# Performance work log

Hardware: AMD Instinct MI355X
Metric: run time of the kernel (lower is better)

## Reference

```python
import jax, jax.numpy as jnp
import numpy as np

DEPTH = 8
INPUT_WIDTH = 64
INNER_WIDTH = 32
BATCH = 65536
N_NODES = 2 ** DEPTH - 1   # 255 inner nodes
N_LEAVES = 2 ** DEPTH      # 256 bins
EPS = 1e-8


def _tree_paths(depth):
    """For each leaf, the inner-node index at each level and whether the path
    goes right (right child uses 1 - decision, mirroring hstack([p, 1-p]) indexing)."""
    node_idx = np.zeros((2 ** depth, depth), dtype=np.int32)
    is_right = np.zeros((2 ** depth, depth), dtype=bool)
    for leaf in range(2 ** depth):
        idx = 0
        for level in range(depth):
            bit = (leaf >> (depth - 1 - level)) & 1
            node_idx[leaf, level] = idx
            is_right[leaf, level] = bool(bit)
            idx = 2 * idx + 1 + bit
    return node_idx, is_right

_NODE_IDX_NP, _IS_RIGHT_NP = _tree_paths(DEPTH)
NODE_IDX = jnp.asarray(_NODE_IDX_NP)   # [L, depth]
IS_RIGHT = jnp.asarray(_IS_RIGHT_NP)   # [L, depth]


def _init_b_i():
    """Replicates PartialRadialLayer.init_tree_weights: thresholds evenly dividing [0,1],
    stored as logits so sigmoid(b_i) recovers the threshold."""
    b = np.zeros(N_NODES, dtype=np.float64)
    b[0] = -0.5
    used = 1
    for i in range(1, DEPTH):
        n_nodes = 2 ** i
        div = float(2 ** (i + 1))
        for node in range(n_nodes):
            b[used + node] = -(2 * node + 1) / div
        used += n_nodes
    return np.log(-b / (1.0 + b)).astype(np.float32).reshape(1, -1)


def setup_inputs() -> dict:
    key = jax.random.key(0)
    kx, kr, kt = jax.random.split(key, 3)
    x = jax.random.normal(kx, (BATCH, INPUT_WIDTH), dtype=jnp.float32)
    # kaiming_normal_ on [1, input_width]: fan_in = input_width
    ray = jax.random.normal(kr, (1, INPUT_WIDTH), dtype=jnp.float32) * np.sqrt(2.0 / INPUT_WIDTH)
    # kaiming_normal_ on [L, I, W]: fan_in = I * W
    inner_transforms = jax.random.normal(kt, (N_LEAVES, INPUT_WIDTH, INNER_WIDTH), dtype=jnp.float32) * np.sqrt(2.0 / (INPUT_WIDTH * INNER_WIDTH))
    w_i = jnp.zeros((1, N_NODES), dtype=jnp.float32)
    a_i = 5.0 * jnp.ones((1, N_NODES), dtype=jnp.float32)
    b_i = jnp.asarray(_init_b_i())
    return {"x": x, "ray": ray, "inner_transforms": inner_transforms,
            "w_i": w_i, "b_i": b_i, "a_i": a_i}


def reference(x, ray, inner_transforms, w_i, b_i, a_i):
    # angles: arccos(cosine_similarity(x, ray)) / pi
    x_norm = jnp.maximum(jnp.linalg.norm(x, axis=1), EPS)            # [B]
    r_norm = jnp.maximum(jnp.linalg.norm(ray, axis=1), EPS)          # [1]
    cos = jnp.clip((x @ ray[0]) / (x_norm * r_norm), -1.0, 1.0)      # [B]
    angles = jnp.arccos(cos) / jnp.pi                                # [B]

    # per-node decisions
    node_fns = (0.5 + jax.nn.sigmoid(w_i)) * angles[:, None] - jax.nn.sigmoid(b_i)  # [B, N]
    decisions = jax.nn.sigmoid(node_fns * (1.0 + a_i))                               # [B, N]

    # soft bin distribution: product along each root-to-leaf path
    g = decisions[:, NODE_IDX]                       # [B, L, depth]
    vals = jnp.where(IS_RIGHT, 1.0 - g, g)           # right child -> 1 - p
    distribution = jnp.prod(vals, axis=2)            # [B, L]

    # weighted per-leaf transforms: einsum('bi,liw->blw') then ('bl,blo->bo'), fused
    out = jnp.einsum('bl,bi,liw->bw', distribution, x, inner_transforms)
    return out
```

## Files before the change

kernel.cpp:

```cpp
#include <hip/hip_runtime.h>
#include <hip/hip_bf16.h>

#define NLEAF 256
#define MBLK 256
#define THREADS 256

typedef __attribute__((ext_vector_type(4))) float f32x4;
typedef __attribute__((ext_vector_type(4))) unsigned int uint4v;
typedef __attribute__((ext_vector_type(8))) __bf16 bf16x8;
typedef __attribute__((ext_vector_type(4))) __bf16 bf16x4;

#define OFF_DIST 0
#define OFF_XP   131072
#define OFF_AC   147456
#define OFF_BC   148480
#define OFF_ANG  149504
#define OFF_RAY  150528
#define SMEM_BYTES 150784

__device__ __forceinline__ float sigf(float s) { return 1.0f / (1.0f + __expf(-s)); }

__global__ __launch_bounds__(256) void prep_T(const float* __restrict__ T,
                                              __bf16* __restrict__ wsT) {
  __shared__ char tile[4096];
  const int l = blockIdx.x;
  const float* src = T + (size_t)l * 2048;
  const int t = threadIdx.x;
#pragma unroll
  for (int p = 0; p < 2; ++p) {
    int e = p * 1024 + t * 4;
    f32x4 v = *(const f32x4*)(src + e);
    int k = e >> 5, w0 = e & 31;
#pragma unroll
    for (int j = 0; j < 4; ++j) {
      int w = w0 + j;
      int off = ((k >> 5) * 2 + (w >> 4)) * 1024 +
                (((k >> 3) & 3) * 16 + (w & 15)) * 16 + (k & 7) * 2;
      *(__bf16*)(tile + off) = (__bf16)v[j];
    }
  }
  __syncthreads();
  *(uint4v*)((char*)wsT + (size_t)l * 4096 + t * 16) = *(const uint4v*)(tile + t * 16);
}

template <bool USE_WS>
__global__ __launch_bounds__(THREADS, 1)
void prl_main(const float* __restrict__ x, const float* __restrict__ ray,
              const float* __restrict__ w_i, const float* __restrict__ b_i,
              const float* __restrict__ a_i, const void* __restrict__ tsrc,
              float* __restrict__ out) {
  extern __shared__ char smem[];
  const int tid = threadIdx.x;
  const int lane = tid & 63;
  const int wid = tid >> 6;
  const int g = lane >> 4;
  const int ln = lane & 15;
  const int row0 = blockIdx.x * MBLK;

  float* A_c = (float*)(smem + OFF_AC);
  float* B_c = (float*)(smem + OFF_BC);
  float* angles = (float*)(smem + OFF_ANG);
  float* ray_l = (float*)(smem + OFF_RAY);
  __bf16* distb = (__bf16*)(smem + OFF_DIST);

  if (tid < 255) {
    float aa = 1.0f + a_i[tid];
    A_c[tid] = (0.5f + sigf(w_i[tid])) * aa;
    B_c[tid] = -sigf(b_i[tid]) * aa;
  }
  if (tid < 64) ray_l[tid] = ray[tid];
  __syncthreads();

  bf16x8 afrag[4][2] = {};
  float* xp = (float*)(smem + OFF_XP);
  for (int c = 0; c < 4; ++c) {
    const float* xg = x + (size_t)(row0 + c * 64) * 64;
#pragma unroll
    for (int p = 0; p < 4; ++p) {
      int idx = p * 256 + tid;
      f32x4 v = *(const f32x4*)(xg + idx * 4);
      *(f32x4*)(xp + idx * 4) = v;
      int cg = idx & 15;
      f32x4 rv = *(const f32x4*)(ray_l + cg * 4);
      float a0 = v[0] * v[0] + v[1] * v[1] + v[2] * v[2] + v[3] * v[3];
      float a1 = v[0] * rv[0] + v[1] * rv[1] + v[2] * rv[2] + v[3] * rv[3];
      float a2 = rv[0] * rv[0] + rv[1] * rv[1] + rv[2] * rv[2] + rv[3] * rv[3];
#pragma unroll
      for (int s = 1; s < 16; s <<= 1) {
        a0 += __shfl_xor(a0, s, 64);
        a1 += __shfl_xor(a1, s, 64);
        a2 += __shfl_xor(a2, s, 64);
      }
      if ((tid & 15) == 0) {
        int r = idx >> 4;
        float xn = fmaxf(sqrtf(a0), 1e-8f);
        float rn = fmaxf(sqrtf(a2), 1e-8f);
        float cs = a1 / (xn * rn);
        cs = fminf(fmaxf(cs, -1.0f), 1.0f);
        angles[c * 64 + r] = acosf(cs) * 0.31830988618379067f;
      }
    }
    __syncthreads();
    if (wid == c) {
#pragma unroll
      for (int mt = 0; mt < 4; ++mt)
#pragma unroll
        for (int kt = 0; kt < 2; ++kt) {
          int rl = mt * 16 + ln;
          int k0 = kt * 32 + g * 8;
          f32x4 u0 = *(const f32x4*)(xp + rl * 64 + k0);
          f32x4 u1 = *(const f32x4*)(xp + rl * 64 + k0 + 4);
          bf16x8 af;
          af[0] = (__bf16)u0[0]; af[1] = (__bf16)u0[1];
          af[2] = (__bf16)u0[2]; af[3] = (__bf16)u0[3];
          af[4] = (__bf16)u1[0]; af[5] = (__bf16)u1[1];
          af[6] = (__bf16)u1[2]; af[7] = (__bf16)u1[3];
          afrag[mt][kt] = af;
        }
    }
    __syncthreads();
  }

  __bf16* PA = (__bf16*)(smem + OFF_XP);
  __bf16* PB = (__bf16*)(smem + OFF_XP + 8192);
  {
    float ang = angles[tid];
    float d = sigf(fmaf(A_c[0], ang, B_c[0]));
    PA[tid] = (__bf16)d;
    PA[256 + tid] = (__bf16)(1.0f - d);
  }
  __syncthreads();
#pragma unroll
  for (int it = 0; it < 2; ++it) {
    int e = it * 256 + tid;
    int n = e >> 8, r = e & 255;
    float p = (float)PA[e];
    float ang = angles[r];
    float d = sigf(fmaf(A_c[1 + n], ang, B_c[1 + n]));
    PB[(2 * n) * 256 + r] = (__bf16)(p * d);
    PB[(2 * n + 1) * 256 + r] = (__bf16)(p * (1.0f - d));
  }
  __syncthreads();
#pragma unroll
  for (int it = 0; it < 4; ++it) {
    int e = it * 256 + tid;
    int n = e >> 8, r = e & 255;
    float p = (float)PB[e];
    float ang = angles[r];
    float d = sigf(fmaf(A_c[3 + n], ang, B_c[3 + n]));
    PA[(2 * n) * 256 + r] = (__bf16)(p * d);
    PA[(2 * n + 1) * 256 + r] = (__bf16)(p * (1.0f - d));
  }
  __syncthreads();
#pragma unroll
  for (int it = 0; it < 8; ++it) {
    int e = it * 256 + tid;
    int n = e >> 8, r = e & 255;
    float p = (float)PA[e];
    float ang = angles[r];
    float d = sigf(fmaf(A_c[7 + n], ang, B_c[7 + n]));
    PB[(2 * n) * 256 + r] = (__bf16)(p * d);
    PB[(2 * n + 1) * 256 + r] = (__bf16)(p * (1.0f - d));
  }
  __syncthreads();
#pragma unroll
  for (int it = 0; it < 16; ++it) {
    int e = it * 256 + tid;
    int n4 = e >> 8, r = e & 255;
    float p4 = (float)PB[e];
    float ang = angles[r];
    float d4 = sigf(fmaf(A_c[15 + n4], ang, B_c[15 + n4]));
    float p5[2] = {p4 * d4, p4 * (1.0f - d4)};
#pragma unroll
    for (int b5 = 0; b5 < 2; ++b5) {
      int n5 = 2 * n4 + b5;
      float d5 = sigf(fmaf(A_c[31 + n5], ang, B_c[31 + n5]));
      float p6[2] = {p5[b5] * d5, p5[b5] * (1.0f - d5)};
#pragma unroll
      for (int b6 = 0; b6 < 2; ++b6) {
        int n6 = 2 * n5 + b6;
        float d6 = sigf(fmaf(A_c[63 + n6], ang, B_c[63 + n6]));
        float p7[2] = {p6[b6] * d6, p6[b6] * (1.0f - d6)};
#pragma unroll
        for (int b7 = 0; b7 < 2; ++b7) {
          int n7 = 2 * n6 + b7;
          float d7 = sigf(fmaf(A_c[127 + n7], ang, B_c[127 + n7]));
          float pv = p7[b7];
          distb[(2 * n7) * 256 + r] = (__bf16)(pv * d7);
          distb[(2 * n7 + 1) * 256 + r] = (__bf16)(pv * (1.0f - d7));
        }
      }
    }
  }
  __syncthreads();

  f32x4 acc[4][2] = {};
  const char* bp = (const char*)tsrc + lane * 16;

  auto step = [&](const bf16x8 (&bv)[4], int l) {
    f32x4 dv[4];
#pragma unroll
    for (int mt = 0; mt < 4; ++mt) {
      bf16x4 dd = *(const bf16x4*)(distb + l * 256 + wid * 64 + mt * 16 + g * 4);
      dv[mt] = (f32x4){(float)dd[0], (float)dd[1], (float)dd[2], (float)dd[3]};
    }
    f32x4 zero = {0.0f, 0.0f, 0.0f, 0.0f};
#pragma unroll
    for (int mt = 0; mt < 4; ++mt)
#pragma unroll
      for (int nt = 0; nt < 2; ++nt) {
        bf16x8 bk0, bk1;
        if constexpr (USE_WS) {
          bk0 = bv[nt];
          bk1 = bv[2 + nt];
        } else {
          const float* tp0 = (const float*)tsrc + (size_t)l * 2048 + (g * 8) * 32 + nt * 16 + ln;
          const float* tp1 = tp0 + 32 * 32;
#pragma unroll
          for (int j = 0; j < 8; ++j) {
            bk0[j] = (__bf16)tp0[j * 32];
            bk1[j] = (__bf16)tp1[j * 32];
          }
        }
        f32x4 y = __builtin_amdgcn_mfma_f32_16x16x32_bf16(afrag[mt][0], bk0, zero, 0, 0, 0);
        y = __builtin_amdgcn_mfma_f32_16x16x32_bf16(afrag[mt][1], bk1, y, 0, 0, 0);
        acc[mt][nt] += dv[mt] * y;
      }
  };

  if constexpr (USE_WS) {
    bf16x8 b0[4], b1[4], b2[4], b3[4];
#pragma unroll
    for (int f = 0; f < 4; ++f) {
      b0[f] = *(const bf16x8*)(bp + 0 * 4096 + f * 1024);
      b1[f] = *(const bf16x8*)(bp + 1 * 4096 + f * 1024);
      b2[f] = *(const bf16x8*)(bp + 2 * 4096 + f * 1024);
      b3[f] = *(const bf16x8*)(bp + 3 * 4096 + f * 1024);
    }
    for (int l = 0; l < NLEAF; l += 4) {
      step(b0, l);
      if (l + 4 < NLEAF) {
        const char* q = bp + (size_t)(l + 4) * 4096;
#pragma unroll
        for (int f = 0; f < 4; ++f) b0[f] = *(const bf16x8*)(q + f * 1024);
      }
      step(b1, l + 1);
      if (l + 5 < NLEAF) {
        const char* q = bp + (size_t)(l + 5) * 4096;
#pragma unroll
        for (int f = 0; f < 4; ++f) b1[f] = *(const bf16x8*)(q + f * 1024);
      }
      step(b2, l + 2);
      if (l + 6 < NLEAF) {
        const char* q = bp + (size_t)(l + 6) * 4096;
#pragma unroll
        for (int f = 0; f < 4; ++f) b2[f] = *(const bf16x8*)(q + f * 1024);
      }
      step(b3, l + 3);
      if (l + 7 < NLEAF) {
        const char* q = bp + (size_t)(l + 7) * 4096;
#pragma unroll
        for (int f = 0; f < 4; ++f) b3[f] = *(const bf16x8*)(q + f * 1024);
      }
    }
  } else {
    bf16x8 dummy[4] = {};
    for (int l = 0; l < NLEAF; ++l) step(dummy, l);
  }

#pragma unroll
  for (int mt = 0; mt < 4; ++mt)
#pragma unroll
    for (int nt = 0; nt < 2; ++nt)
#pragma unroll
      for (int e = 0; e < 4; ++e) {
        int row = row0 + wid * 64 + mt * 16 + g * 4 + e;
        out[(size_t)row * 32 + nt * 16 + ln] = acc[mt][nt][e];
      }
}

extern "C" void kernel_launch(void* const* d_in, const int* in_sizes, int n_in,
                              void* d_out, int out_size, void* d_ws, size_t ws_size,
                              hipStream_t stream) {
  const float* x = (const float*)d_in[0];
  const float* ray = (const float*)d_in[1];
  const float* T = (const float*)d_in[2];
  const float* w_i = (const float*)d_in[3];
  const float* b_i = (const float*)d_in[4];
  const float* a_i = (const float*)d_in[5];
  float* out = (float*)d_out;

  bool use_ws = ws_size >= (size_t)NLEAF * 4096;
  if (use_ws) {
    hipFuncSetAttribute(reinterpret_cast<const void*>(&prl_main<true>),
                        hipFuncAttributeMaxDynamicSharedMemorySize, SMEM_BYTES);
    prep_T<<<256, 256, 0, stream>>>(T, (__bf16*)d_ws);
    prl_main<true><<<256, THREADS, SMEM_BYTES, stream>>>(x, ray, w_i, b_i, a_i, d_ws, out);
  } else {
    hipFuncSetAttribute(reinterpret_cast<const void*>(&prl_main<false>),
                        hipFuncAttributeMaxDynamicSharedMemorySize, SMEM_BYTES);
    prl_main<false><<<256, THREADS, SMEM_BYTES, stream>>>(x, ray, w_i, b_i, a_i, T, out);
  }
}
```

Baseline: 188.8 us.

## Stage leaf transforms through double-buffered LDS with 8 waves splitting output columns

Doubles the block to 512 threads, with waves split into row groups and column halves, so each wave computes a 64x16 output tile instead of 64x32. The per-leaf transform tiles are now loaded cooperatively into a double-buffered, XOR-swizzled LDS region, replacing per-wave register prefetch straight from global memory. The distribution rows are permuted so that each lane reads its weights with two 16-byte LDS loads. This removes redundant global loads across waves and adds occupancy, at the cost of a block-wide barrier every two leaves.

```diff
diff --git a/kernel.cpp b/kernel.cpp
--- a/kernel.cpp
+++ b/kernel.cpp
@@ -3,7 +3,7 @@
 
 #define NLEAF 256
 #define MBLK 256
-#define THREADS 256
+#define THREADS 512
 
 typedef __attribute__((ext_vector_type(4))) float f32x4;
 typedef __attribute__((ext_vector_type(4))) unsigned int uint4v;
@@ -20,6 +20,10 @@
 
 __device__ __forceinline__ float sigf(float s) { return 1.0f / (1.0f + __expf(-s)); }
 
+__device__ __forceinline__ int permr(int r) {
+  return (r & 0xC3) | ((r & 0x30) >> 2) | ((r & 0x0C) << 2);
+}
+
 __global__ __launch_bounds__(256) void prep_T(const float* __restrict__ T,
                                               __bf16* __restrict__ wsT) {
   __shared__ char tile[4096];
@@ -34,8 +38,7 @@
 #pragma unroll
     for (int j = 0; j < 4; ++j) {
       int w = w0 + j;
-      int off = ((k >> 5) * 2 + (w >> 4)) * 1024 +
-                (((k >> 3) & 3) * 16 + (w & 15)) * 16 + (k & 7) * 2;
+      int off = (w * 128 + 2 * k) ^ ((w & 7) << 4);
       *(__bf16*)(tile + off) = (__bf16)v[j];
     }
   }
@@ -44,7 +47,7 @@
 }
 
 template <bool USE_WS>
-__global__ __launch_bounds__(THREADS, 1)
+__global__ __launch_bounds__(THREADS, 2)
 void prl_main(const float* __restrict__ x, const float* __restrict__ ray,
               const float* __restrict__ w_i, const float* __restrict__ b_i,
               const float* __restrict__ a_i, const void* __restrict__ tsrc,
@@ -53,6 +56,8 @@
   const int tid = threadIdx.x;
   const int lane = tid & 63;
   const int wid = tid >> 6;
+  const int rg = wid >> 1;
+  const int cg = wid & 1;
   const int g = lane >> 4;
   const int ln = lane & 15;
   const int row0 = blockIdx.x * MBLK;
@@ -68,7 +73,7 @@
     A_c[tid] = (0.5f + sigf(w_i[tid])) * aa;
     B_c[tid] = -sigf(b_i[tid]) * aa;
   }
-  if (tid < 64) ray_l[tid] = ray[tid];
+  if (tid >= 256 && tid < 320) ray_l[tid - 256] = ray[tid - 256];
   __syncthreads();
 
   bf16x8 afrag[4][2] = {};
@@ -76,12 +81,12 @@
   for (int c = 0; c < 4; ++c) {
     const float* xg = x + (size_t)(row0 + c * 64) * 64;
 #pragma unroll
-    for (int p = 0; p < 4; ++p) {
-      int idx = p * 256 + tid;
+    for (int p = 0; p < 2; ++p) {
+      int idx = p * 512 + tid;
       f32x4 v = *(const f32x4*)(xg + idx * 4);
       *(f32x4*)(xp + idx * 4) = v;
-      int cg = idx & 15;
-      f32x4 rv = *(const f32x4*)(ray_l + cg * 4);
+      int cgr = idx & 15;
+      f32x4 rv = *(const f32x4*)(ray_l + cgr * 4);
       float a0 = v[0] * v[0] + v[1] * v[1] + v[2] * v[2] + v[3] * v[3];
       float a1 = v[0] * rv[0] + v[1] * rv[1] + v[2] * rv[2] + v[3] * rv[3];
       float a2 = rv[0] * rv[0] + rv[1] * rv[1] + rv[2] * rv[2] + rv[3] * rv[3];
@@ -101,7 +106,7 @@
       }
     }
     __syncthreads();
-    if (wid == c) {
+    if (rg == c) {
 #pragma unroll
       for (int mt = 0; mt < 4; ++mt)
 #pragma unroll
@@ -123,18 +128,16 @@
 
   __bf16* PA = (__bf16*)(smem + OFF_XP);
   __bf16* PB = (__bf16*)(smem + OFF_XP + 8192);
-  {
+  if (tid < 256) {
     float ang = angles[tid];
     float d = sigf(fmaf(A_c[0], ang, B_c[0]));
     PA[tid] = (__bf16)d;
     PA[256 + tid] = (__bf16)(1.0f - d);
   }
   __syncthreads();
-#pragma unroll
-  for (int it = 0; it < 2; ++it) {
-    int e = it * 256 + tid;
-    int n = e >> 8, r = e & 255;
-    float p = (float)PA[e];
+  {
+    int n = tid >> 8, r = tid & 255;
+    float p = (float)PA[tid];
     float ang = angles[r];
     float d = sigf(fmaf(A_c[1 + n], ang, B_c[1 + n]));
     PB[(2 * n) * 256 + r] = (__bf16)(p * d);
@@ -142,8 +145,8 @@
   }
   __syncthreads();
 #pragma unroll
-  for (int it = 0; it < 4; ++it) {
-    int e = it * 256 + tid;
+  for (int it = 0; it < 2; ++it) {
+    int e = it * 512 + tid;
     int n = e >> 8, r = e & 255;
     float p = (float)PB[e];
     float ang = angles[r];
@@ -153,8 +156,8 @@
   }
   __syncthreads();
 #pragma unroll
-  for (int it = 0; it < 8; ++it) {
-    int e = it * 256 + tid;
+  for (int it = 0; it < 4; ++it) {
+    int e = it * 512 + tid;
     int n = e >> 8, r = e & 255;
     float p = (float)PA[e];
     float ang = angles[r];
@@ -163,120 +166,105 @@
     PB[(2 * n + 1) * 256 + r] = (__bf16)(p * (1.0f - d));
   }
   __syncthreads();
-#pragma unroll
-  for (int it = 0; it < 16; ++it) {
-    int e = it * 256 + tid;
-    int n4 = e >> 8, r = e & 255;
-    float p4 = (float)PB[e];
-    float ang = angles[r];
-    float d4 = sigf(fmaf(A_c[15 + n4], ang, B_c[15 + n4]));
-    float p5[2] = {p4 * d4, p4 * (1.0f - d4)};
-#pragma unroll
-    for (int b5 = 0; b5 < 2; ++b5) {
-      int n5 = 2 * n4 + b5;
-      float d5 = sigf(fmaf(A_c[31 + n5], ang, B_c[31 + n5]));
-      float p6[2] = {p5[b5] * d5, p5[b5] * (1.0f - d5)};
-#pragma unroll
-      for (int b6 = 0; b6 < 2; ++b6) {
-        int n6 = 2 * n5 + b6;
-        float d6 = sigf(fmaf(A_c[63 + n6], ang, B_c[63 + n6]));
-        float p7[2] = {p6[b6] * d6, p6[b6] * (1.0f - d6)};
-#pragma unroll
-        for (int b7 = 0; b7 < 2; ++b7) {
-          int n7 = 2 * n6 + b7;
-          float d7 = sigf(fmaf(A_c[127 + n7], ang, B_c[127 + n7]));
-          float pv = p7[b7];
-          distb[(2 * n7) * 256 + r] = (__bf16)(pv * d7);
-          distb[(2 * n7 + 1) * 256 + r] = (__bf16)(pv * (1.0f - d7));
-        }
-      }
-    }
-  }
-  __syncthreads();
-
-  f32x4 acc[4][2] = {};
-  const char* bp = (const char*)tsrc + lane * 16;
-
-  auto step = [&](const bf16x8 (&bv)[4], int l) {
-    f32x4 dv[4];
-#pragma unroll
-    for (int mt = 0; mt < 4; ++mt) {
-      bf16x4 dd = *(const bf16x4*)(distb + l * 256 + wid * 64 + mt * 16 + g * 4);
-      dv[mt] = (f32x4){(float)dd[0], (float)dd[1], (float)dd[2], (float)dd[3]};
-    }
-    f32x4 zero = {0.0f, 0.0f, 0.0f, 0.0f};
-#pragma unroll
-    for (int mt = 0; mt < 4; ++mt)
-#pragma unroll
-      for (int nt = 0; nt < 2; ++nt) {
-        bf16x8 bk0, bk1;
-        if constexpr (USE_WS) {
-          bk0 = bv[nt];
-          bk1 = bv[2 + nt];
-        } else {
-          const float* tp0 = (const float*)tsrc + (size_t)l * 2048 + (g * 8) * 32 + nt * 16 + ln;
-          const float* tp1 = tp0 + 32 * 32;
-#pragma unroll
-          for (int j = 0; j < 8; ++j) {
-            bk0[j] = (__bf16)tp0[j * 32];
-            bk1[j] = (__bf16)tp1[j * 32];
+  {
+    const int r = tid & 255;
+    const int pr = permr(r);
+    const float ang = angles[r];
+#pragma unroll
+    for (int it = 0; it < 8; ++it) {
+      int n4 = it * 2 + (tid >> 8);
+      float p4 = (float)PB[n4 * 256 + r];
+      float d4 = sigf(fmaf(A_c[15 + n4], ang, B_c[15 + n4]));
+      float p5[2] = {p4 * d4, p4 * (1.0f - d4)};
+#pragma unroll
+      for (int b5 = 0; b5 < 2; ++b5) {
+        int n5 = 2 * n4 + b5;
+        float d5 = sigf(fmaf(A_c[31 + n5], ang, B_c[31 + n5]));
+        float p6[2] = {p5[b5] * d5, p5[b5] * (1.0f - d5)};
+#pragma unroll
+        for (int b6 = 0; b6 < 2; ++b6) {
+          int n6 = 2 * n5 + b6;
+          float d6 = sigf(fmaf(A_c[63 + n6], ang, B_c[63 + n6]));
+          float p7[2] = {p6[b6] * d6, p6[b6] * (1.0f - d6)};
+#pragma unroll
+          for (int b7 = 0; b7 < 2; ++b7) {
+            int n7 = 2 * n6 + b7;
+            float d7 = sigf(fmaf(A_c[127 + n7], ang, B_c[127 + n7]));
+            float pv = p7[b7];
+            distb[(2 * n7) * 256 + pr] = (__bf16)(pv * d7);
+            distb[(2 * n7 + 1) * 256 + pr] = (__bf16)(pv * (1.0f - d7));
           }
         }
-        f32x4 y = __builtin_amdgcn_mfma_f32_16x16x32_bf16(afrag[mt][0], bk0, zero, 0, 0, 0);
-        y = __builtin_amdgcn_mfma_f32_16x16x32_bf16(afrag[mt][1], bk1, y, 0, 0, 0);
-        acc[mt][nt] += dv[mt] * y;
-      }
+      }
+    }
+  }
+  __syncthreads();
+
+  f32x4 acc[4] = {};
+  const int wB = cg * 16 + ln;
+  const int ad0 = (wB * 128 + g * 16) ^ ((wB & 7) << 4);
+  const int ad1 = (wB * 128 + 64 + g * 16) ^ ((wB & 7) << 4);
+
+  auto compute = [&](bf16x8 bk0, bf16x8 bk1, int l) {
+    const __bf16* dp = distb + l * 256 + rg * 64 + g * 16;
+    bf16x8 q0 = *(const bf16x8*)dp;
+    bf16x8 q1 = *(const bf16x8*)(dp + 8);
+    f32x4 dv[4];
+    dv[0] = (f32x4){(float)q0[0], (float)q0[1], (float)q0[2], (float)q0[3]};
+    dv[1] = (f32x4){(float)q0[4], (float)q0[5], (float)q0[6], (float)q0[7]};
+    dv[2] = (f32x4){(float)q1[0], (float)q1[1], (float)q1[2], (float)q1[3]};
+    dv[3] = (f32x4){(float)q1[4], (float)q1[5], (float)q1[6], (float)q1[7]};
+    f32x4 zero = {0.0f, 0.0f, 0.0f, 0.0f};
+#pragma unroll
+    for (int mt = 0; mt < 4; ++mt) {
+      f32x4 y = __builtin_amdgcn_mfma_f32_16x16x32_bf16(afrag[mt][0], bk0, zero, 0, 0, 0);
+      y = __builtin_amdgcn_mfma_f32_16x16x32_bf16(afrag[mt][1], bk1, y, 0, 0, 0);
+      acc[mt] += dv[mt] * y;
+    }
   };
 
+  char* tb = smem + OFF_XP;
+
   if constexpr (USE_WS) {
-    bf16x8 b0[4], b1[4], b2[4], b3[4];
-#pragma unroll
-    for (int f = 0; f < 4; ++f) {
-      b0[f] = *(const bf16x8*)(bp + 0 * 4096 + f * 1024);
-      b1[f] = *(const bf16x8*)(bp + 1 * 4096 + f * 1024);
-      b2[f] = *(const bf16x8*)(bp + 2 * 4096 + f * 1024);
-      b3[f] = *(const bf16x8*)(bp + 3 * 4096 + f * 1024);
-    }
-    for (int l = 0; l < NLEAF; l += 4) {
-      step(b0, l);
-      if (l + 4 < NLEAF) {
-        const char* q = bp + (size_t)(l + 4) * 4096;
-#pragma unroll
-        for (int f = 0; f < 4; ++f) b0[f] = *(const bf16x8*)(q + f * 1024);
-      }
-      step(b1, l + 1);
-      if (l + 5 < NLEAF) {
-        const char* q = bp + (size_t)(l + 5) * 4096;
-#pragma unroll
-        for (int f = 0; f < 4; ++f) b1[f] = *(const bf16x8*)(q + f * 1024);
-      }
-      step(b2, l + 2);
-      if (l + 6 < NLEAF) {
-        const char* q = bp + (size_t)(l + 6) * 4096;
-#pragma unroll
-        for (int f = 0; f < 4; ++f) b2[f] = *(const bf16x8*)(q + f * 1024);
-      }
-      step(b3, l + 3);
-      if (l + 7 < NLEAF) {
-        const char* q = bp + (size_t)(l + 7) * 4096;
-#pragma unroll
-        for (int f = 0; f < 4; ++f) b3[f] = *(const bf16x8*)(q + f * 1024);
-      }
+    const int ts = tid >> 8;
+    const int to = (tid & 255) * 16;
+    uint4v tv = *(const uint4v*)((const char*)tsrc + ts * 4096 + to);
+    *(uint4v*)(tb + ts * 4096 + to) = tv;
+    tv = *(const uint4v*)((const char*)tsrc + (2 + ts) * 4096 + to);
+    __syncthreads();
+    for (int l = 0; l < NLEAF; l += 2) {
+      char* cur = tb + ((l >> 1) & 1) * 8192;
+      char* nxt = tb + (((l >> 1) + 1) & 1) * 8192;
+      if (l + 2 < NLEAF) {
+        *(uint4v*)(nxt + ts * 4096 + to) = tv;
+        if (l + 4 < NLEAF)
+          tv = *(const uint4v*)((const char*)tsrc + (size_t)(l + 4 + ts) * 4096 + to);
+      }
+      compute(*(const bf16x8*)(cur + ad0), *(const bf16x8*)(cur + ad1), l);
+      compute(*(const bf16x8*)(cur + 4096 + ad0), *(const bf16x8*)(cur + 4096 + ad1), l + 1);
+      __syncthreads();
     }
   } else {
-    bf16x8 dummy[4] = {};
-    for (int l = 0; l < NLEAF; ++l) step(dummy, l);
+    for (int l = 0; l < NLEAF; ++l) {
+      const float* tp0 = (const float*)tsrc + (size_t)l * 2048 + (g * 8) * 32 + wB;
+      const float* tp1 = tp0 + 32 * 32;
+      bf16x8 bk0, bk1;
+#pragma unroll
+      for (int j = 0; j < 8; ++j) {
+        bk0[j] = (__bf16)tp0[j * 32];
+        bk1[j] = (__bf16)tp1[j * 32];
+      }
+      compute(bk0, bk1, l);
+    }
   }
 
 #pragma unroll
   for (int mt = 0; mt < 4; ++mt)
 #pragma unroll
-    for (int nt = 0; nt < 2; ++nt)
-#pragma unroll
-      for (int e = 0; e < 4; ++e) {
-        int row = row0 + wid * 64 + mt * 16 + g * 4 + e;
-        out[(size_t)row * 32 + nt * 16 + ln] = acc[mt][nt][e];
-      }
+    for (int e = 0; e < 4; ++e) {
+      int row = row0 + rg * 64 + mt * 16 + g * 4 + e;
+      out[(size_t)row * 32 + cg * 16 + ln] = acc[mt][e];
+    }
 }
 
 extern "C" void kernel_launch(void* const* d_in, const int* in_sizes, int n_in,
```

New measurement: 174.6 us. 1.08x faster.
